# Kernel optimization log

Measured on AMD Instinct MI355X. Metric: run time of the kernel, lower is better.

The kernel has to match this reference:

```python
import jax, jax.numpy as jnp
import numpy as np

FORMULA_OH_SIZES = [20, 20, 20, 20, 20]
SPECT_BIN_N = 512


def layer_norm(x, g, b, eps=1e-5):
    m = jnp.mean(x, axis=-1, keepdims=True)
    v = jnp.var(x, axis=-1, keepdims=True)
    return (x - m) * jax.lax.rsqrt(v + eps) * g + b


def gru_cell(x, h, W_ih, W_hh, b_ih, b_hh):
    # torch.nn.GRUCell math
    gi = x @ W_ih.T + b_ih
    gh = h @ W_hh.T + b_hh
    i_r, i_z, i_n = jnp.split(gi, 3, axis=-1)
    h_r, h_z, h_n = jnp.split(gh, 3, axis=-1)
    r = jax.nn.sigmoid(i_r + h_r)
    z = jax.nn.sigmoid(i_z + h_z)
    n = jnp.tanh(i_n + r * h_n)
    return (1.0 - z) * n + z * h


def structured_one_hot(x, sizes, accum=True):
    # x: [N, len(sizes)] integer element counts -> concatenated (accumulated) one-hots
    outs = []
    for i, s in enumerate(sizes):
        v = jnp.clip(x[:, i].astype(jnp.int32), 0, s - 1)
        if accum:
            oh = (jnp.arange(s)[None, :] <= v[:, None]).astype(jnp.float32)  # thermometer
        else:
            oh = jax.nn.one_hot(v, s, dtype=jnp.float32)
        outs.append(oh)
    return jnp.concatenate(outs, axis=-1)


def setup_inputs():
    key = jax.random.key(0)
    ks = jax.random.split(key, 16)
    B, A, GF, HW, S, M = 16, 32, 128, 4, 4096, 8
    G = GF * HW                       # 512 = g_feat_in * highway_steps_n
    FE = sum(FORMULA_OH_SIZES)        # 100
    D = 512                           # internal_d
    vert_feat_in = jax.random.normal(ks[0], (B, A, GF, HW), jnp.float32)
    vert_mask_in = jnp.ones((B, A), jnp.float32)
    elem_id = jax.random.randint(ks[1], (B, A), 0, 5)
    vert_element_oh = jax.nn.one_hot(elem_id, 5, dtype=jnp.float32)
    adj_oh = jnp.zeros((B, A, A, 4), jnp.float32)  # unused by forward
    atom_subsets = jax.random.bernoulli(ks[2], 0.5, (B, S, A)).astype(jnp.float32)
    masses = jax.random.uniform(ks[3], (B, S, M), jnp.float32, 0.0, SPECT_BIN_N - 1.0)
    intens = jax.random.uniform(ks[4], (B, S, M), jnp.float32)
    atom_subsets_peaks = jnp.stack([masses, intens], axis=-1)

    def lin(k, o, i):
        return (jax.random.normal(k, (o, i), jnp.float32) / np.sqrt(i)).astype(jnp.float32)

    return dict(
        vert_feat_in=vert_feat_in, vert_mask_in=vert_mask_in,
        vert_element_oh=vert_element_oh, adj_oh=adj_oh,
        atom_subsets=atom_subsets, atom_subsets_peaks=atom_subsets_peaks,
        ln_sub_g=jnp.ones((G,), jnp.float32), ln_sub_b=jnp.zeros((G,), jnp.float32),
        W_ih=lin(ks[5], 3 * G, FE), W_hh=lin(ks[6], 3 * G, G),
        b_ih=jnp.zeros((3 * G,), jnp.float32), b_hh=jnp.zeros((3 * G,), jnp.float32),
        W1=lin(ks[7], D, G), b1=jnp.zeros((D,), jnp.float32),
        W2a=lin(ks[8], D, D), b2a=jnp.zeros((D,), jnp.float32),
        W2b=lin(ks[9], D, D), b2b=jnp.zeros((D,), jnp.float32),
        ln_pre_g=jnp.ones((D,), jnp.float32), ln_pre_b=jnp.zeros((D,), jnp.float32),
        Ws=lin(ks[10], 1, D), bs=jnp.zeros((1,), jnp.float32),
    )


def reference(vert_feat_in, vert_mask_in, vert_element_oh, adj_oh, atom_subsets,
              atom_subsets_peaks, ln_sub_g, ln_sub_b, W_ih, W_hh, b_ih, b_hh,
              W1, b1, W2a, b2a, W2b, b2b, ln_pre_g, ln_pre_b, Ws, bs):
    B, A, GF, HW = vert_feat_in.shape
    S = atom_subsets.shape[1]
    vf = vert_feat_in.reshape(B, A, GF * HW)                       # [B,A,G]
    masked_vf = vf * vert_mask_in[:, :, None]
    subs_m = atom_subsets * vert_mask_in[:, None, :]               # [B,S,A]
    swvs = jnp.einsum('bag,bsa->bsg', masked_vf, subs_m)           # [B,S,G]
    # per-subset element counts -> structured one-hot formula encoding
    counts = jnp.einsum('bae,bsa->bse', vert_element_oh, atom_subsets).astype(jnp.int32)
    pf_flat = structured_one_hot(counts.reshape(B * S, -1), FORMULA_OH_SIZES, accum=True)
    subset_size = jnp.sum(subs_m, axis=2) + 1e-4                   # [B,S]
    mean = swvs / subset_size[:, :, None]
    normed = layer_norm(mean, ln_sub_g, ln_sub_b)                  # [B,S,G]
    h = gru_cell(pf_flat, normed.reshape(B * S, -1), W_ih, W_hh, b_ih, b_hh)
    h = h.reshape(normed.shape)
    x = jax.nn.relu(h @ W1.T + b1)
    x = jax.nn.relu(x @ W2a.T + b2a)
    x = jax.nn.relu(x @ W2b.T + b2b)   # (extra F.relu in original is idempotent)
    x = layer_norm(x, ln_pre_g, ln_pre_b)
    scores = (x @ Ws.T + bs)[..., 0]                               # [B,S]
    probs = jax.nn.softmax(scores, axis=-1)
    # mass histogram: scatter intensity*prob into rounded-mass bins
    masses = atom_subsets_peaks[..., 0]                            # [B,S,M]
    intens = atom_subsets_peaks[..., 1]
    bins = jnp.clip(jnp.round(masses).astype(jnp.int32), 0, SPECT_BIN_N - 1)
    contrib = intens * probs[:, :, None]                           # [B,S,M]
    spect = jnp.zeros((B, SPECT_BIN_N), x.dtype).at[
        jnp.arange(B)[:, None], bins.reshape(B, -1)].add(contrib.reshape(B, -1))
    return (spect, probs)
```

## Files before the change

### kernel.cpp

```cpp
#include <hip/hip_runtime.h>
#include <math.h>

#define B_ 16
#define A_ 32
#define G_ 512
#define S_ 4096
#define M_ 8
#define BS_ 65536
#define KC_ 640
#define NG_ 1536

typedef _Float16 half8 __attribute__((ext_vector_type(8)));
typedef _Float16 half4v __attribute__((ext_vector_type(4)));
typedef _Float16 half2v __attribute__((ext_vector_type(2)));
typedef float floatx4 __attribute__((ext_vector_type(4)));

typedef const __attribute__((address_space(1))) void* gas_t;
typedef __attribute__((address_space(3))) void* las_t;

__device__ __forceinline__ float wave_sum_f(float v){
#pragma unroll
  for (int o = 32; o > 0; o >>= 1) v += __shfl_xor(v, o);
  return v;
}
__device__ __forceinline__ float wave_max_f(float v){
#pragma unroll
  for (int o = 32; o > 0; o >>= 1) v = fmaxf(v, __shfl_xor(v, o));
  return v;
}
__device__ __forceinline__ float sigmoidf_(float x){ return 1.f/(1.f+__expf(-x)); }
__device__ __forceinline__ float tanhf_(float x){ return 1.f - 2.f/(__expf(2.f*x)+1.f); }

__global__ __launch_bounds__(256) void k_cvt3(const float* __restrict__ s0,
                                              const float* __restrict__ s1,
                                              const float* __restrict__ s2,
                                              _Float16* __restrict__ d){
  const float* s = (blockIdx.y == 0) ? s0 : (blockIdx.y == 1) ? s1 : s2;
  int i = (blockIdx.x*256 + threadIdx.x)*4;
  if (i >= G_*G_) return;
  float4 v = *(const float4*)(s+i);
  half4v o; o[0]=(_Float16)v.x; o[1]=(_Float16)v.y; o[2]=(_Float16)v.z; o[3]=(_Float16)v.w;
  *(half4v*)(d + (size_t)blockIdx.y*G_*G_ + i) = o;
}

__global__ __launch_bounds__(64) void k_buildw(const float* __restrict__ Whh,
                                               const float* __restrict__ Wih,
                                               _Float16* __restrict__ Wcat){
  int j = blockIdx.x;
  for (int p = threadIdx.x; p < KC_; p += 64){
    float v = 0.f;
    if (p < 512) v = Whh[(size_t)j*512 + p];
    else if (p < 612) v = Wih[(size_t)j*100 + (p - 512)];
    Wcat[(size_t)j*KC_ + p] = (_Float16)v;
  }
}

__global__ __launch_bounds__(256) void k_prep_mfma(
    const float* __restrict__ vf, const float* __restrict__ mask,
    const float* __restrict__ eoh, const float* __restrict__ subs,
    const float* __restrict__ ln_g, const float* __restrict__ ln_b,
    _Float16* __restrict__ Abuf){
  __shared__ _Float16 s_mvfT[G_*A_];
  __shared__ _Float16 s_sm[128*A_];
  __shared__ float s_m[A_];
  __shared__ float s_e[A_*5];
  __shared__ float s_ssum[128];
  __shared__ float s_red1[2][4][16];
  __shared__ float s_red2[2][4][16];
  int tid = threadIdx.x;
  int bx = blockIdx.x, b = blockIdx.y;
  int lane = tid & 63, w = tid >> 6;
  int q = lane >> 4, l15 = lane & 15;
  size_t row0 = (size_t)b*S_ + (size_t)bx*128;
  if (tid < A_)   s_m[tid] = mask[b*A_ + tid];
  if (tid < A_*5) s_e[tid] = eoh[b*A_*5 + tid];
  __syncthreads();
  {
    int p = tid & 15, gseg = tid >> 4;
    float mk0 = s_m[2*p], mk1 = s_m[2*p+1];
    const float* v0 = vf + ((size_t)b*A_ + 2*p)*G_ + gseg*32;
    const float* v1 = v0 + G_;
#pragma unroll
    for (int i = 0; i < 32; i += 4){
      float4 a = *(const float4*)(v0 + i);
      float4 c = *(const float4*)(v1 + i);
      float av[4] = {a.x, a.y, a.z, a.w};
      float cv[4] = {c.x, c.y, c.z, c.w};
#pragma unroll
      for (int j = 0; j < 4; ++j){
        half2v h; h[0] = (_Float16)(av[j]*mk0); h[1] = (_Float16)(cv[j]*mk1);
        *(half2v*)(s_mvfT + (gseg*32 + i + j)*A_ + 2*p) = h;
      }
    }
  }
  {
    int s = tid >> 1, hh = tid & 1;
    const float* sp = subs + (row0 + s)*A_ + hh*16;
    _Float16* dst = s_sm + s*A_ + hh*16;
#pragma unroll
    for (int i = 0; i < 16; i += 4){
      float4 v = *(const float4*)(sp + i);
      half4v h; h[0]=(_Float16)v.x; h[1]=(_Float16)v.y; h[2]=(_Float16)v.z; h[3]=(_Float16)v.w;
      *(half4v*)(dst + i) = h;
    }
  }
  __syncthreads();
  if (tid < 128){
    int s = tid;
    float ssum = 0.f, c0=0.f, c1=0.f, c2=0.f, c3=0.f, c4=0.f;
#pragma unroll
    for (int a = 0; a < A_; ++a){
      float v = (float)s_sm[s*A_ + a];
      ssum += v * s_m[a];
      c0 += v * s_e[a*5+0]; c1 += v * s_e[a*5+1]; c2 += v * s_e[a*5+2];
      c3 += v * s_e[a*5+3]; c4 += v * s_e[a*5+4];
    }
    int cc[5];
    cc[0] = min(max((int)(c0+0.5f),0),19); cc[1] = min(max((int)(c1+0.5f),0),19);
    cc[2] = min(max((int)(c2+0.5f),0),19); cc[3] = min(max((int)(c3+0.5f),0),19);
    cc[4] = min(max((int)(c4+0.5f),0),19);
    s_ssum[s] = ssum;
    _Float16* dst = Abuf + (row0 + s)*KC_ + 512;
#pragma unroll
    for (int t = 0; t < 16; ++t){
      half8 hv;
#pragma unroll
      for (int u = 0; u < 8; ++u){
        int k = t*8 + u;
        float v = 0.f;
        if (k < 100){ int f = k/20, l = k - f*20; v = (l <= cc[f]) ? 1.f : 0.f; }
        hv[u] = (_Float16)v;
      }
      *(half8*)(dst + t*8) = hv;
    }
  }
  half8 bf[8]; float lng[8], lnb[8];
#pragma unroll
  for (int t = 0; t < 8; ++t){
    int g = w*128 + t*16 + l15;
    bf[t] = *(const half8*)(s_mvfT + g*A_ + q*8);
    lng[t] = ln_g[g]; lnb[t] = ln_b[g];
  }
  __syncthreads();
  for (int gi = 0; gi < 8; ++gi){
    half8 af = *(const half8*)(s_sm + (gi*16 + l15)*A_ + q*8);
    floatx4 c[8];
#pragma unroll
    for (int t = 0; t < 8; ++t){
      floatx4 z = {0.f, 0.f, 0.f, 0.f};
      c[t] = __builtin_amdgcn_mfma_f32_16x16x32_f16(af, bf[t], z, 0, 0, 0);
    }
    float p1[4] = {0.f,0.f,0.f,0.f}, p2[4] = {0.f,0.f,0.f,0.f};
#pragma unroll
    for (int t = 0; t < 8; ++t)
#pragma unroll
      for (int r = 0; r < 4; ++r){ float v = c[t][r]; p1[r] += v; p2[r] += v*v; }
#pragma unroll
    for (int off = 1; off < 16; off <<= 1)
#pragma unroll
      for (int r = 0; r < 4; ++r){
        p1[r] += __shfl_xor(p1[r], off);
        p2[r] += __shfl_xor(p2[r], off);
      }
    int gb = gi & 1;
    if (l15 == 0){
#pragma unroll
      for (int r = 0; r < 4; ++r){ s_red1[gb][w][q*4+r] = p1[r]; s_red2[gb][w][q*4+r] = p2[r]; }
    }
    __syncthreads();
#pragma unroll
    for (int r = 0; r < 4; ++r){
      int sl = gi*16 + q*4 + r;
      int rr = q*4 + r;
      float t1 = s_red1[gb][0][rr] + s_red1[gb][1][rr] + s_red1[gb][2][rr] + s_red1[gb][3][rr];
      float t2 = s_red2[gb][0][rr] + s_red2[gb][1][rr] + s_red2[gb][2][rr] + s_red2[gb][3][rr];
      float inv = 1.f/(s_ssum[sl] + 1e-4f);
      float mu = t1*inv*(1.f/512.f);
      float var = t2*inv*inv*(1.f/512.f) - mu*mu;
      float rs = rsqrtf(var + 1e-5f);
      _Float16* orow = Abuf + (row0 + sl)*KC_;
#pragma unroll
      for (int t = 0; t < 8; ++t){
        float o = (c[t][r]*inv - mu)*rs*lng[t] + lnb[t];
        orow[w*128 + t*16 + l15] = (_Float16)o;
      }
    }
  }
}

__global__ __launch_bounds__(512) void k_gru_fused(
    const _Float16* __restrict__ Abuf, const _Float16* __restrict__ Wcat,
    const float* __restrict__ bih, const float* __restrict__ bhh,
    _Float16* __restrict__ H){
  __shared__ _Float16 smA[2][128*32];
  __shared__ _Float16 smB[2][192*32];
  int tid = threadIdx.x;
  int lane = tid & 63, wvid = tid >> 6;
  int wm = wvid & 1, wn = wvid >> 1;
  int q = lane >> 4, l15 = lane & 15;
  int mt = blockIdx.x*64 + (blockIdx.y >> 3);
  int dt = blockIdx.y & 7;
  int m0 = mt*128, n0 = dt*64;
  floatx4 acc[3][4] = {};
  floatx4 accNI[4] = {};
  int offA[4], offB[3];
#pragma unroll
  for (int i = 0; i < 4; ++i){
    int r = wm*64 + i*16 + l15;
    offA[i] = (r*4 + (q ^ ((r>>2)&3)))*8;
  }
#pragma unroll
  for (int g = 0; g < 3; ++g){
    int rb = g*64 + wn*16 + l15;
    offB[g] = (rb*4 + (q ^ ((rb>>2)&3)))*8;
  }
  const _Float16* gA;
  {
    int u = wvid*64 + lane;
    int r = u >> 2, c = (u & 3) ^ ((r >> 2) & 3);
    gA = Abuf + (size_t)(m0 + r)*KC_ + c*8;
  }
  const _Float16* gB0;
  {
    int u = wvid*64 + lane;
    int rb = u >> 2, c = (u & 3) ^ ((rb >> 2) & 3);
    int grow = (rb >> 6)*512 + n0 + (rb & 63);
    gB0 = Wcat + (size_t)grow*KC_ + c*8;
  }
  const _Float16* gB1 = nullptr;
  if (wvid < 4){
    int u = (8 + wvid)*64 + lane;
    int rb = u >> 2, c = (u & 3) ^ ((rb >> 2) & 3);
    int grow = (rb >> 6)*512 + n0 + (rb & 63);
    gB1 = Wcat + (size_t)grow*KC_ + c*8;
  }
  __builtin_amdgcn_global_load_lds((gas_t)gA,  (las_t)(smA[0] + wvid*512), 16, 0, 0);
  __builtin_amdgcn_global_load_lds((gas_t)gB0, (las_t)(smB[0] + wvid*512), 16, 0, 0);
  if (wvid < 4)
    __builtin_amdgcn_global_load_lds((gas_t)gB1, (las_t)(smB[0] + (8+wvid)*512), 16, 0, 0);
  asm volatile("s_waitcnt vmcnt(0)");
  __builtin_amdgcn_s_barrier();
  const int NT = KC_/32;
  for (int t = 0; t < NT; ++t){
    int cur = t & 1;
    if (t + 1 < NT){
      int kc = (t+1)*32;
      __builtin_amdgcn_global_load_lds((gas_t)(gA + kc),  (las_t)(smA[cur^1] + wvid*512), 16, 0, 0);
      __builtin_amdgcn_global_load_lds((gas_t)(gB0 + kc), (las_t)(smB[cur^1] + wvid*512), 16, 0, 0);
      if (wvid < 4)
        __builtin_amdgcn_global_load_lds((gas_t)(gB1 + kc), (las_t)(smB[cur^1] + (8+wvid)*512), 16, 0, 0);
    }
    half8 af[4], bfv[3];
#pragma unroll
    for (int i = 0; i < 4; ++i) af[i] = *(const half8*)(smA[cur] + offA[i]);
#pragma unroll
    for (int g = 0; g < 3; ++g) bfv[g] = *(const half8*)(smB[cur] + offB[g]);
    if (t < 16){
#pragma unroll
      for (int g = 0; g < 3; ++g)
#pragma unroll
        for (int i = 0; i < 4; ++i)
          acc[g][i] = __builtin_amdgcn_mfma_f32_16x16x32_f16(af[i], bfv[g], acc[g][i], 0, 0, 0);
    } else {
#pragma unroll
      for (int i = 0; i < 4; ++i){
        acc[0][i] = __builtin_amdgcn_mfma_f32_16x16x32_f16(af[i], bfv[0], acc[0][i], 0, 0, 0);
        acc[1][i] = __builtin_amdgcn_mfma_f32_16x16x32_f16(af[i], bfv[1], acc[1][i], 0, 0, 0);
        accNI[i]  = __builtin_amdgcn_mfma_f32_16x16x32_f16(af[i], bfv[2], accNI[i], 0, 0, 0);
      }
    }
    asm volatile("s_waitcnt vmcnt(0)");
    __builtin_amdgcn_s_barrier();
  }
  int d = n0 + wn*16 + l15;
  float br  = bih[d] + bhh[d];
  float bz  = bih[512+d] + bhh[512+d];
  float bnh = bhh[1024+d];
  float bni = bih[1024+d];
#pragma unroll
  for (int i = 0; i < 4; ++i){
#pragma unroll
    for (int r = 0; r < 4; ++r){
      int m = m0 + wm*64 + i*16 + q*4 + r;
      float gr  = acc[0][i][r] + br;
      float gz  = acc[1][i][r] + bz;
      float hn  = acc[2][i][r] + bnh;
      float in_ = accNI[i][r] + bni;
      float rrv = sigmoidf_(gr);
      float zz  = sigmoidf_(gz);
      float nn  = tanhf_(in_ + rrv*hn);
      float hp  = (float)Abuf[(size_t)m*KC_ + d];
      H[(size_t)m*G_ + d] = (_Float16)((1.f-zz)*nn + zz*hp);
    }
  }
}

__global__ __launch_bounds__(256) void k_gemm(
    const _Float16* __restrict__ A, const _Float16* __restrict__ W,
    const float* __restrict__ bias, _Float16* __restrict__ Out){
  __shared__ _Float16 smA[2][128*32];
  __shared__ _Float16 smB[2][128*32];
  int tid = threadIdx.x;
  int lane = tid & 63, wvid = tid >> 6;
  int wm = wvid & 1, wn = wvid >> 1;
  int q = lane >> 4, l15 = lane & 15;
  int mt = blockIdx.x*64 + (blockIdx.y >> 2);
  int nt = blockIdx.y & 3;
  int m0 = mt*128, n0 = nt*128;
  floatx4 acc[4][4] = {};
  int offA[4], offB[4];
#pragma unroll
  for (int i = 0; i < 4; ++i){
    int r = wm*64 + i*16 + l15;
    offA[i] = (r*4 + (q ^ ((r>>2)&3)))*8;
    int rb = wn*64 + i*16 + l15;
    offB[i] = (rb*4 + (q ^ ((rb>>2)&3)))*8;
  }
  int uA[2];
  const _Float16 *gA[2], *gB[2];
#pragma unroll
  for (int t = 0; t < 2; ++t){
    int seg = wvid*2 + t;
    int u = seg*64 + lane;
    int r = u >> 2, c = (u & 3) ^ ((r >> 2) & 3);
    uA[t] = seg;
    gA[t] = A + (size_t)(m0 + r)*G_ + c*8;
    gB[t] = W + (size_t)(n0 + r)*G_ + c*8;
  }
#pragma unroll
  for (int t2 = 0; t2 < 2; ++t2){
    __builtin_amdgcn_global_load_lds((gas_t)(gA[t2]), (las_t)(smA[0] + uA[t2]*512), 16, 0, 0);
    __builtin_amdgcn_global_load_lds((gas_t)(gB[t2]), (las_t)(smB[0] + uA[t2]*512), 16, 0, 0);
  }
  asm volatile("s_waitcnt vmcnt(0)");
  __builtin_amdgcn_s_barrier();
  const int NT = G_/32;
  for (int t = 0; t < NT; ++t){
    int cur = t & 1;
    if (t + 1 < NT){
      int kc = (t+1)*32;
#pragma unroll
      for (int t2 = 0; t2 < 2; ++t2){
        __builtin_amdgcn_global_load_lds((gas_t)(gA[t2] + kc), (las_t)(smA[cur^1] + uA[t2]*512), 16, 0, 0);
        __builtin_amdgcn_global_load_lds((gas_t)(gB[t2] + kc), (las_t)(smB[cur^1] + uA[t2]*512), 16, 0, 0);
      }
    }
    half8 af[4], bfv[4];
#pragma unroll
    for (int i = 0; i < 4; ++i) af[i] = *(const half8*)(smA[cur] + offA[i]);
#pragma unroll
    for (int j = 0; j < 4; ++j) bfv[j] = *(const half8*)(smB[cur] + offB[j]);
#pragma unroll
    for (int i = 0; i < 4; ++i)
#pragma unroll
      for (int j = 0; j < 4; ++j)
        acc[i][j] = __builtin_amdgcn_mfma_f32_16x16x32_f16(af[i], bfv[j], acc[i][j], 0, 0, 0);
    asm volatile("s_waitcnt vmcnt(0)");
    __builtin_amdgcn_s_barrier();
  }
#pragma unroll
  for (int j = 0; j < 4; ++j){
    int n = n0 + wn*64 + j*16 + l15;
    float bv = bias[n];
#pragma unroll
    for (int i = 0; i < 4; ++i){
#pragma unroll
      for (int r = 0; r < 4; ++r){
        int m = m0 + wm*64 + i*16 + q*4 + r;
        Out[(size_t)m*G_ + n] = (_Float16)fmaxf(acc[i][j][r] + bv, 0.f);
      }
    }
  }
}

__global__ __launch_bounds__(256) void k_ff3_fin(
    const _Float16* __restrict__ A, const _Float16* __restrict__ W,
    const float* __restrict__ bias, const float* __restrict__ ln_pre_g,
    const float* __restrict__ Ws, float* __restrict__ Pbuf){
  __shared__ _Float16 smA[2][128*32];
  __shared__ _Float16 smB[2][128*32];
  __shared__ float sP[2][64][2][3];
  int tid = threadIdx.x;
  int lane = tid & 63, wvid = tid >> 6;
  int wm = wvid & 1, wn = wvid >> 1;
  int q = lane >> 4, l15 = lane & 15;
  int mt = blockIdx.x*64 + (blockIdx.y >> 2);
  int nt = blockIdx.y & 3;
  int m0 = mt*128, n0 = nt*128;
  floatx4 acc[4][4] = {};
  int offA[4], offB[4];
#pragma unroll
  for (int i = 0; i < 4; ++i){
    int r = wm*64 + i*16 + l15;
    offA[i] = (r*4 + (q ^ ((r>>2)&3)))*8;
    int rb = wn*64 + i*16 + l15;
    offB[i] = (rb*4 + (q ^ ((rb>>2)&3)))*8;
  }
  int uA[2];
  const _Float16 *gA[2], *gB[2];
#pragma unroll
  for (int t = 0; t < 2; ++t){
    int seg = wvid*2 + t;
    int u = seg*64 + lane;
    int r = u >> 2, c = (u & 3) ^ ((r >> 2) & 3);
    uA[t] = seg;
    gA[t] = A + (size_t)(m0 + r)*G_ + c*8;
    gB[t] = W + (size_t)(n0 + r)*G_ + c*8;
  }
#pragma unroll
  for (int t2 = 0; t2 < 2; ++t2){
    __builtin_amdgcn_global_load_lds((gas_t)(gA[t2]), (las_t)(smA[0] + uA[t2]*512), 16, 0, 0);
    __builtin_amdgcn_global_load_lds((gas_t)(gB[t2]), (las_t)(smB[0] + uA[t2]*512), 16, 0, 0);
  }
  asm volatile("s_waitcnt vmcnt(0)");
  __builtin_amdgcn_s_barrier();
  const int NT = G_/32;
  for (int t = 0; t < NT; ++t){
    int cur = t & 1;
    if (t + 1 < NT){
      int kc = (t+1)*32;
#pragma unroll
      for (int t2 = 0; t2 < 2; ++t2){
        __builtin_amdgcn_global_load_lds((gas_t)(gA[t2] + kc), (las_t)(smA[cur^1] + uA[t2]*512), 16, 0, 0);
        __builtin_amdgcn_global_load_lds((gas_t)(gB[t2] + kc), (las_t)(smB[cur^1] + uA[t2]*512), 16, 0, 0);
      }
    }
    half8 af[4], bfv[4];
#pragma unroll
    for (int i = 0; i < 4; ++i) af[i] = *(const half8*)(smA[cur] + offA[i]);
#pragma unroll
    for (int j = 0; j < 4; ++j) bfv[j] = *(const half8*)(smB[cur] + offB[j]);
#pragma unroll
    for (int i = 0; i < 4; ++i)
#pragma unroll
      for (int j = 0; j < 4; ++j)
        acc[i][j] = __builtin_amdgcn_mfma_f32_16x16x32_f16(af[i], bfv[j], acc[i][j], 0, 0, 0);
    asm volatile("s_waitcnt vmcnt(0)");
    __builtin_amdgcn_s_barrier();
  }
  float gws[4], bv4[4];
#pragma unroll
  for (int j = 0; j < 4; ++j){
    int n = n0 + wn*64 + j*16 + l15;
    gws[j] = ln_pre_g[n]*Ws[n];
    bv4[j] = bias[n];
  }
#pragma unroll
  for (int i = 0; i < 4; ++i){
#pragma unroll
    for (int r = 0; r < 4; ++r){
      float p1 = 0.f, p2 = 0.f, p3 = 0.f;
#pragma unroll
      for (int j = 0; j < 4; ++j){
        float x = fmaxf(acc[i][j][r] + bv4[j], 0.f);
        p1 += x; p2 += x*x; p3 += gws[j]*x;
      }
#pragma unroll
      for (int off = 1; off < 16; off <<= 1){
        p1 += __shfl_xor(p1, off);
        p2 += __shfl_xor(p2, off);
        p3 += __shfl_xor(p3, off);
      }
      if (l15 == 0){
        int rl = i*16 + q*4 + r;
        sP[wm][rl][wn][0] = p1; sP[wm][rl][wn][1] = p2; sP[wm][rl][wn][2] = p3;
      }
    }
  }
  __syncthreads();
  if (tid < 128){
    int wmi = tid >> 6, rl = tid & 63;
    int m = m0 + wmi*64 + rl;
    float* dst = Pbuf + ((size_t)m*4 + nt)*3;
    dst[0] = sP[wmi][rl][0][0] + sP[wmi][rl][1][0];
    dst[1] = sP[wmi][rl][0][1] + sP[wmi][rl][1][1];
    dst[2] = sP[wmi][rl][0][2] + sP[wmi][rl][1][2];
  }
}

__global__ __launch_bounds__(256) void k_score_fin(
    const float* __restrict__ Pbuf, const float* __restrict__ g,
    const float* __restrict__ bta, const float* __restrict__ Ws,
    const float* __restrict__ bs, float* __restrict__ scores){
  __shared__ float red[8];
  int tid = threadIdx.x, lane = tid & 63, wv = tid >> 6;
  int i0 = tid*2;
  float c1p = g[i0]*Ws[i0] + g[i0+1]*Ws[i0+1];
  float c2p = bta[i0]*Ws[i0] + bta[i0+1]*Ws[i0+1];
  c1p = wave_sum_f(c1p); c2p = wave_sum_f(c2p);
  if (lane == 0){ red[wv] = c1p; red[4+wv] = c2p; }
  __syncthreads();
  float c1 = red[0]+red[1]+red[2]+red[3];
  float c2 = red[4]+red[5]+red[6]+red[7] + bs[0];
  size_t row = (size_t)blockIdx.x*256 + tid;
  const float* p = Pbuf + row*12;
  float4 a  = *(const float4*)p;
  float4 b4 = *(const float4*)(p+4);
  float4 c4 = *(const float4*)(p+8);
  float P1 = a.x + a.w + b4.z + c4.y;
  float P2 = a.y + b4.x + b4.w + c4.z;
  float P3 = a.z + b4.y + c4.x + c4.w;
  float mu = P1*(1.f/512.f);
  float var = P2*(1.f/512.f) - mu*mu;
  float rs = rsqrtf(var + 1e-5f);
  scores[row] = rs*(P3 - mu*c1) + c2;
}

__global__ __launch_bounds__(256) void k_softmax(
    const float* __restrict__ scores, float* __restrict__ probs){
  __shared__ float red[4];
  int b = blockIdx.x, tid = threadIdx.x, lane = tid & 63, wv = tid >> 6;
  const float* sp = scores + (size_t)b*S_;
  float mx = -1e30f;
  for (int i = tid; i < S_; i += 256) mx = fmaxf(mx, sp[i]);
  mx = wave_max_f(mx);
  if (lane == 0) red[wv] = mx;
  __syncthreads();
  mx = fmaxf(fmaxf(red[0], red[1]), fmaxf(red[2], red[3]));
  __syncthreads();
  float sum = 0.f;
  for (int i = tid; i < S_; i += 256) sum += __expf(sp[i]-mx);
  sum = wave_sum_f(sum);
  if (lane == 0) red[wv] = sum;
  __syncthreads();
  sum = red[0]+red[1]+red[2]+red[3];
  float inv = 1.f/sum;
  for (int i = tid; i < S_; i += 256)
    probs[(size_t)b*S_ + i] = __expf(sp[i]-mx)*inv;
}

__global__ __launch_bounds__(256) void k_spect(
    const float* __restrict__ peaks, const float* __restrict__ probs,
    float* __restrict__ spect){
  __shared__ float bins[512];
  int b = blockIdx.x, tid = threadIdx.x;
  bins[tid] = 0.f; bins[tid+256] = 0.f;
  __syncthreads();
  for (int i = tid; i < S_*M_; i += 256){
    int s = i >> 3, m = i & 7;
    const float* pk = peaks + (((size_t)b*S_ + s)*M_ + m)*2;
    float mass = pk[0], inten = pk[1];
    float p = probs[(size_t)b*S_ + s];
    int bin = (int)rintf(mass);
    bin = min(max(bin, 0), 511);
    atomicAdd(&bins[bin], inten*p);
  }
  __syncthreads();
  spect[(size_t)b*512 + tid]       = bins[tid];
  spect[(size_t)b*512 + tid + 256] = bins[tid+256];
}

extern "C" void kernel_launch(void* const* d_in, const int* in_sizes, int n_in,
                              void* d_out, int out_size, void* d_ws, size_t ws_size,
                              hipStream_t stream) {
  const float* vf       = (const float*)d_in[0];
  const float* mask     = (const float*)d_in[1];
  const float* eoh      = (const float*)d_in[2];
  const float* subs     = (const float*)d_in[4];
  const float* peaks    = (const float*)d_in[5];
  const float* ln_sub_g = (const float*)d_in[6];
  const float* ln_sub_b = (const float*)d_in[7];
  const float* W_ih     = (const float*)d_in[8];
  const float* W_hh     = (const float*)d_in[9];
  const float* b_ih     = (const float*)d_in[10];
  const float* b_hh     = (const float*)d_in[11];
  const float* W1       = (const float*)d_in[12];
  const float* b1       = (const float*)d_in[13];
  const float* W2a      = (const float*)d_in[14];
  const float* b2a      = (const float*)d_in[15];
  const float* W2b      = (const float*)d_in[16];
  const float* b2b      = (const float*)d_in[17];
  const float* ln_pre_g = (const float*)d_in[18];
  const float* ln_pre_b = (const float*)d_in[19];
  const float* Ws       = (const float*)d_in[20];
  const float* bs       = (const float*)d_in[21];
  float* out = (float*)d_out;
  float* probs_out = out + (size_t)B_*512;

  char* w = (char*)d_ws;
  float* scores = (float*)w;     w += (size_t)BS_*4;
  float* Pbuf   = (float*)w;     w += (size_t)BS_*12*4;
  _Float16* Wcat = (_Float16*)w; w += (size_t)NG_*KC_*2;
  _Float16* W1h  = (_Float16*)w; w += (size_t)G_*G_*2;
  _Float16* W2ah = (_Float16*)w; w += (size_t)G_*G_*2;
  _Float16* W2bh = (_Float16*)w; w += (size_t)G_*G_*2;
  _Float16* Abuf = (_Float16*)w; w += (size_t)BS_*KC_*2;
  _Float16* bufh0 = (_Float16*)w;
  _Float16* bufh1 = Abuf;

  k_cvt3<<<dim3((G_*G_/4+255)/256, 3), 256, 0, stream>>>(W1, W2a, W2b, W1h);
  k_buildw<<<NG_, 64, 0, stream>>>(W_hh, W_ih, Wcat);
  k_prep_mfma<<<dim3(S_/128, B_), 256, 0, stream>>>(vf, mask, eoh, subs,
                                                    ln_sub_g, ln_sub_b, Abuf);
  k_gru_fused<<<dim3(8, 512), 512, 0, stream>>>(Abuf, Wcat, b_ih, b_hh, bufh0);
  k_gemm<<<dim3(8, 256), 256, 0, stream>>>(bufh0, W1h,  b1,  bufh1);
  k_gemm<<<dim3(8, 256), 256, 0, stream>>>(bufh1, W2ah, b2a, bufh0);
  k_ff3_fin<<<dim3(8, 256), 256, 0, stream>>>(bufh0, W2bh, b2b,
                                              ln_pre_g, Ws, Pbuf);
  k_score_fin<<<BS_/256, 256, 0, stream>>>(Pbuf, ln_pre_g, ln_pre_b, Ws, bs, scores);
  k_softmax<<<B_, 256, 0, stream>>>(scores, probs_out);
  k_spect<<<B_, 256, 0, stream>>>(peaks, probs_out, out);
}
```

Measured before the change: 525.8 us.

## Triple-buffer LDS tiles with partial vmcnt waits in GRU and FF GEMMs

```diff
diff --git a/kernel.cpp b/kernel.cpp
--- a/kernel.cpp
+++ b/kernel.cpp
@@ -192,8 +192,8 @@
     const _Float16* __restrict__ Abuf, const _Float16* __restrict__ Wcat,
     const float* __restrict__ bih, const float* __restrict__ bhh,
     _Float16* __restrict__ H){
-  __shared__ _Float16 smA[2][128*32];
-  __shared__ _Float16 smB[2][192*32];
+  __shared__ _Float16 smA[3][128*32];
+  __shared__ _Float16 smB[3][192*32];
   int tid = threadIdx.x;
   int lane = tid & 63, wvid = tid >> 6;
   int wm = wvid & 1, wn = wvid >> 1;
@@ -234,22 +234,26 @@
     int grow = (rb >> 6)*512 + n0 + (rb & 63);
     gB1 = Wcat + (size_t)grow*KC_ + c*8;
   }
-  __builtin_amdgcn_global_load_lds((gas_t)gA,  (las_t)(smA[0] + wvid*512), 16, 0, 0);
-  __builtin_amdgcn_global_load_lds((gas_t)gB0, (las_t)(smB[0] + wvid*512), 16, 0, 0);
-  if (wvid < 4)
-    __builtin_amdgcn_global_load_lds((gas_t)gB1, (las_t)(smB[0] + (8+wvid)*512), 16, 0, 0);
-  asm volatile("s_waitcnt vmcnt(0)");
-  __builtin_amdgcn_s_barrier();
+#define GRU_STAGE(TT, BUF) do{                                                        \
+    int kc_ = (TT)*32;                                                                \
+    __builtin_amdgcn_global_load_lds((gas_t)(gA + kc_),  (las_t)(smA[BUF] + wvid*512), 16, 0, 0); \
+    __builtin_amdgcn_global_load_lds((gas_t)(gB0 + kc_), (las_t)(smB[BUF] + wvid*512), 16, 0, 0); \
+    if (wvid < 4)                                                                     \
+      __builtin_amdgcn_global_load_lds((gas_t)(gB1 + kc_), (las_t)(smB[BUF] + (8+wvid)*512), 16, 0, 0); \
+  }while(0)
+  GRU_STAGE(0, 0);
+  GRU_STAGE(1, 1);
   const int NT = KC_/32;
   for (int t = 0; t < NT; ++t){
-    int cur = t & 1;
-    if (t + 1 < NT){
-      int kc = (t+1)*32;
-      __builtin_amdgcn_global_load_lds((gas_t)(gA + kc),  (las_t)(smA[cur^1] + wvid*512), 16, 0, 0);
-      __builtin_amdgcn_global_load_lds((gas_t)(gB0 + kc), (las_t)(smB[cur^1] + wvid*512), 16, 0, 0);
-      if (wvid < 4)
-        __builtin_amdgcn_global_load_lds((gas_t)(gB1 + kc), (las_t)(smB[cur^1] + (8+wvid)*512), 16, 0, 0);
-    }
+    int cur = t % 3;
+    if (t < NT-1){
+      if (wvid < 4) asm volatile("s_waitcnt vmcnt(3)" ::: "memory");
+      else          asm volatile("s_waitcnt vmcnt(2)" ::: "memory");
+    } else {
+      asm volatile("s_waitcnt vmcnt(0)" ::: "memory");
+    }
+    __builtin_amdgcn_s_barrier();
+    if (t + 2 < NT) GRU_STAGE(t+2, (t+2)%3);
     half8 af[4], bfv[3];
 #pragma unroll
     for (int i = 0; i < 4; ++i) af[i] = *(const half8*)(smA[cur] + offA[i]);
@@ -269,9 +273,8 @@
         accNI[i]  = __builtin_amdgcn_mfma_f32_16x16x32_f16(af[i], bfv[2], accNI[i], 0, 0, 0);
       }
     }
-    asm volatile("s_waitcnt vmcnt(0)");
-    __builtin_amdgcn_s_barrier();
-  }
+  }
+#undef GRU_STAGE
   int d = n0 + wn*16 + l15;
   float br  = bih[d] + bhh[d];
   float bz  = bih[512+d] + bhh[512+d];
@@ -298,8 +301,8 @@
 __global__ __launch_bounds__(256) void k_gemm(
     const _Float16* __restrict__ A, const _Float16* __restrict__ W,
     const float* __restrict__ bias, _Float16* __restrict__ Out){
-  __shared__ _Float16 smA[2][128*32];
-  __shared__ _Float16 smB[2][128*32];
+  __shared__ _Float16 smA[3][128*32];
+  __shared__ _Float16 smB[3][128*32];
   int tid = threadIdx.x;
   int lane = tid & 63, wvid = tid >> 6;
   int wm = wvid & 1, wn = wvid >> 1;
@@ -327,24 +330,22 @@
     gA[t] = A + (size_t)(m0 + r)*G_ + c*8;
     gB[t] = W + (size_t)(n0 + r)*G_ + c*8;
   }
-#pragma unroll
-  for (int t2 = 0; t2 < 2; ++t2){
-    __builtin_amdgcn_global_load_lds((gas_t)(gA[t2]), (las_t)(smA[0] + uA[t2]*512), 16, 0, 0);
-    __builtin_amdgcn_global_load_lds((gas_t)(gB[t2]), (las_t)(smB[0] + uA[t2]*512), 16, 0, 0);
-  }
-  asm volatile("s_waitcnt vmcnt(0)");
-  __builtin_amdgcn_s_barrier();
+#define FF_STAGE(TT, BUF) do{                                                         \
+    int kc_ = (TT)*32;                                                                \
+    __builtin_amdgcn_global_load_lds((gas_t)(gA[0] + kc_), (las_t)(smA[BUF] + uA[0]*512), 16, 0, 0); \
+    __builtin_amdgcn_global_load_lds((gas_t)(gB[0] + kc_), (las_t)(smB[BUF] + uA[0]*512), 16, 0, 0); \
+    __builtin_amdgcn_global_load_lds((gas_t)(gA[1] + kc_), (las_t)(smA[BUF] + uA[1]*512), 16, 0, 0); \
+    __builtin_amdgcn_global_load_lds((gas_t)(gB[1] + kc_), (las_t)(smB[BUF] + uA[1]*512), 16, 0, 0); \
+  }while(0)
+  FF_STAGE(0, 0);
+  FF_STAGE(1, 1);
   const int NT = G_/32;
   for (int t = 0; t < NT; ++t){
-    int cur = t & 1;
-    if (t + 1 < NT){
-      int kc = (t+1)*32;
-#pragma unroll
-      for (int t2 = 0; t2 < 2; ++t2){
-        __builtin_amdgcn_global_load_lds((gas_t)(gA[t2] + kc), (las_t)(smA[cur^1] + uA[t2]*512), 16, 0, 0);
-        __builtin_amdgcn_global_load_lds((gas_t)(gB[t2] + kc), (las_t)(smB[cur^1] + uA[t2]*512), 16, 0, 0);
-      }
-    }
+    int cur = t % 3;
+    if (t < NT-1) asm volatile("s_waitcnt vmcnt(4)" ::: "memory");
+    else          asm volatile("s_waitcnt vmcnt(0)" ::: "memory");
+    __builtin_amdgcn_s_barrier();
+    if (t + 2 < NT) FF_STAGE(t+2, (t+2)%3);
     half8 af[4], bfv[4];
 #pragma unroll
     for (int i = 0; i < 4; ++i) af[i] = *(const half8*)(smA[cur] + offA[i]);
@@ -355,9 +356,8 @@
 #pragma unroll
       for (int j = 0; j < 4; ++j)
         acc[i][j] = __builtin_amdgcn_mfma_f32_16x16x32_f16(af[i], bfv[j], acc[i][j], 0, 0, 0);
-    asm volatile("s_waitcnt vmcnt(0)");
-    __builtin_amdgcn_s_barrier();
-  }
+  }
+#undef FF_STAGE
 #pragma unroll
   for (int j = 0; j < 4; ++j){
     int n = n0 + wn*64 + j*16 + l15;
@@ -377,8 +377,8 @@
     const _Float16* __restrict__ A, const _Float16* __restrict__ W,
     const float* __restrict__ bias, const float* __restrict__ ln_pre_g,
     const float* __restrict__ Ws, float* __restrict__ Pbuf){
-  __shared__ _Float16 smA[2][128*32];
-  __shared__ _Float16 smB[2][128*32];
+  __shared__ _Float16 smA[3][128*32];
+  __shared__ _Float16 smB[3][128*32];
   __shared__ float sP[2][64][2][3];
   int tid = threadIdx.x;
   int lane = tid & 63, wvid = tid >> 6;
@@ -407,24 +407,22 @@
     gA[t] = A + (size_t)(m0 + r)*G_ + c*8;
     gB[t] = W + (size_t)(n0 + r)*G_ + c*8;
   }
-#pragma unroll
-  for (int t2 = 0; t2 < 2; ++t2){
-    __builtin_amdgcn_global_load_lds((gas_t)(gA[t2]), (las_t)(smA[0] + uA[t2]*512), 16, 0, 0);
-    __builtin_amdgcn_global_load_lds((gas_t)(gB[t2]), (las_t)(smB[0] + uA[t2]*512), 16, 0, 0);
-  }
-  asm volatile("s_waitcnt vmcnt(0)");
-  __builtin_amdgcn_s_barrier();
+#define FF_STAGE(TT, BUF) do{                                                         \
+    int kc_ = (TT)*32;                                                                \
+    __builtin_amdgcn_global_load_lds((gas_t)(gA[0] + kc_), (las_t)(smA[BUF] + uA[0]*512), 16, 0, 0); \
+    __builtin_amdgcn_global_load_lds((gas_t)(gB[0] + kc_), (las_t)(smB[BUF] + uA[0]*512), 16, 0, 0); \
+    __builtin_amdgcn_global_load_lds((gas_t)(gA[1] + kc_), (las_t)(smA[BUF] + uA[1]*512), 16, 0, 0); \
+    __builtin_amdgcn_global_load_lds((gas_t)(gB[1] + kc_), (las_t)(smB[BUF] + uA[1]*512), 16, 0, 0); \
+  }while(0)
+  FF_STAGE(0, 0);
+  FF_STAGE(1, 1);
   const int NT = G_/32;
   for (int t = 0; t < NT; ++t){
-    int cur = t & 1;
-    if (t + 1 < NT){
-      int kc = (t+1)*32;
-#pragma unroll
-      for (int t2 = 0; t2 < 2; ++t2){
-        __builtin_amdgcn_global_load_lds((gas_t)(gA[t2] + kc), (las_t)(smA[cur^1] + uA[t2]*512), 16, 0, 0);
-        __builtin_amdgcn_global_load_lds((gas_t)(gB[t2] + kc), (las_t)(smB[cur^1] + uA[t2]*512), 16, 0, 0);
-      }
-    }
+    int cur = t % 3;
+    if (t < NT-1) asm volatile("s_waitcnt vmcnt(4)" ::: "memory");
+    else          asm volatile("s_waitcnt vmcnt(0)" ::: "memory");
+    __builtin_amdgcn_s_barrier();
+    if (t + 2 < NT) FF_STAGE(t+2, (t+2)%3);
     half8 af[4], bfv[4];
 #pragma unroll
     for (int i = 0; i < 4; ++i) af[i] = *(const half8*)(smA[cur] + offA[i]);
@@ -435,9 +433,8 @@
 #pragma unroll
       for (int j = 0; j < 4; ++j)
         acc[i][j] = __builtin_amdgcn_mfma_f32_16x16x32_f16(af[i], bfv[j], acc[i][j], 0, 0, 0);
-    asm volatile("s_waitcnt vmcnt(0)");
-    __builtin_amdgcn_s_barrier();
-  }
+  }
+#undef FF_STAGE
   float gws[4], bv4[4];
 #pragma unroll
   for (int j = 0; j < 4; ++j){
```

Result: slower. 649.9 us (+23.6%).

## Enlarge feed-forward GEMM tiles to 256x128 with eight waves per block

Applied to the files above, without the earlier changes.

```diff
diff --git a/kernel.cpp b/kernel.cpp
--- a/kernel.cpp
+++ b/kernel.cpp
@@ -295,18 +295,18 @@
   }
 }
 
-__global__ __launch_bounds__(256) void k_gemm(
+__global__ __launch_bounds__(512, 4) void k_gemm(
     const _Float16* __restrict__ A, const _Float16* __restrict__ W,
     const float* __restrict__ bias, _Float16* __restrict__ Out){
-  __shared__ _Float16 smA[2][128*32];
+  __shared__ _Float16 smA[2][256*32];
   __shared__ _Float16 smB[2][128*32];
   int tid = threadIdx.x;
   int lane = tid & 63, wvid = tid >> 6;
-  int wm = wvid & 1, wn = wvid >> 1;
+  int wm = wvid & 3, wn = wvid >> 2;
   int q = lane >> 4, l15 = lane & 15;
-  int mt = blockIdx.x*64 + (blockIdx.y >> 2);
+  int mt = blockIdx.x*32 + (blockIdx.y >> 2);
   int nt = blockIdx.y & 3;
-  int m0 = mt*128, n0 = nt*128;
+  int m0 = mt*256, n0 = nt*128;
   floatx4 acc[4][4] = {};
   int offA[4], offB[4];
 #pragma unroll
@@ -316,35 +316,34 @@
     int rb = wn*64 + i*16 + l15;
     offB[i] = (rb*4 + (q ^ ((rb>>2)&3)))*8;
   }
-  int uA[2];
-  const _Float16 *gA[2], *gB[2];
+  int segA[2];
+  const _Float16 *gA[2], *gB;
 #pragma unroll
   for (int t = 0; t < 2; ++t){
     int seg = wvid*2 + t;
     int u = seg*64 + lane;
     int r = u >> 2, c = (u & 3) ^ ((r >> 2) & 3);
-    uA[t] = seg;
+    segA[t] = seg;
     gA[t] = A + (size_t)(m0 + r)*G_ + c*8;
-    gB[t] = W + (size_t)(n0 + r)*G_ + c*8;
-  }
-#pragma unroll
-  for (int t2 = 0; t2 < 2; ++t2){
-    __builtin_amdgcn_global_load_lds((gas_t)(gA[t2]), (las_t)(smA[0] + uA[t2]*512), 16, 0, 0);
-    __builtin_amdgcn_global_load_lds((gas_t)(gB[t2]), (las_t)(smB[0] + uA[t2]*512), 16, 0, 0);
-  }
+  }
+  {
+    int u = wvid*64 + lane;
+    int rb = u >> 2, c = (u & 3) ^ ((rb >> 2) & 3);
+    gB = W + (size_t)(n0 + rb)*G_ + c*8;
+  }
+#define FF_STAGE(TT, BUF) do{                                                         \
+    int kc_ = (TT)*32;                                                                \
+    __builtin_amdgcn_global_load_lds((gas_t)(gA[0] + kc_), (las_t)(smA[BUF] + segA[0]*512), 16, 0, 0); \
+    __builtin_amdgcn_global_load_lds((gas_t)(gA[1] + kc_), (las_t)(smA[BUF] + segA[1]*512), 16, 0, 0); \
+    __builtin_amdgcn_global_load_lds((gas_t)(gB    + kc_), (las_t)(smB[BUF] + wvid*512), 16, 0, 0);    \
+  }while(0)
+  FF_STAGE(0, 0);
   asm volatile("s_waitcnt vmcnt(0)");
   __builtin_amdgcn_s_barrier();
   const int NT = G_/32;
   for (int t = 0; t < NT; ++t){
     int cur = t & 1;
-    if (t + 1 < NT){
-      int kc = (t+1)*32;
-#pragma unroll
-      for (int t2 = 0; t2 < 2; ++t2){
-        __builtin_amdgcn_global_load_lds((gas_t)(gA[t2] + kc), (las_t)(smA[cur^1] + uA[t2]*512), 16, 0, 0);
-        __builtin_amdgcn_global_load_lds((gas_t)(gB[t2] + kc), (las_t)(smB[cur^1] + uA[t2]*512), 16, 0, 0);
-      }
-    }
+    if (t + 1 < NT) FF_STAGE(t+1, cur^1);
     half8 af[4], bfv[4];
 #pragma unroll
     for (int i = 0; i < 4; ++i) af[i] = *(const half8*)(smA[cur] + offA[i]);
@@ -358,6 +357,7 @@
     asm volatile("s_waitcnt vmcnt(0)");
     __builtin_amdgcn_s_barrier();
   }
+#undef FF_STAGE
 #pragma unroll
   for (int j = 0; j < 4; ++j){
     int n = n0 + wn*64 + j*16 + l15;
@@ -373,20 +373,20 @@
   }
 }
 
-__global__ __launch_bounds__(256) void k_ff3_fin(
+__global__ __launch_bounds__(512, 4) void k_ff3_fin(
     const _Float16* __restrict__ A, const _Float16* __restrict__ W,
     const float* __restrict__ bias, const float* __restrict__ ln_pre_g,
     const float* __restrict__ Ws, float* __restrict__ Pbuf){
-  __shared__ _Float16 smA[2][128*32];
+  __shared__ _Float16 smA[2][256*32];
   __shared__ _Float16 smB[2][128*32];
-  __shared__ float sP[2][64][2][3];
+  __shared__ float sP[4][64][2][3];
   int tid = threadIdx.x;
   int lane = tid & 63, wvid = tid >> 6;
-  int wm = wvid & 1, wn = wvid >> 1;
+  int wm = wvid & 3, wn = wvid >> 2;
   int q = lane >> 4, l15 = lane & 15;
-  int mt = blockIdx.x*64 + (blockIdx.y >> 2);
+  int mt = blockIdx.x*32 + (blockIdx.y >> 2);
   int nt = blockIdx.y & 3;
-  int m0 = mt*128, n0 = nt*128;
+  int m0 = mt*256, n0 = nt*128;
   floatx4 acc[4][4] = {};
   int offA[4], offB[4];
 #pragma unroll
@@ -396,35 +396,34 @@
     int rb = wn*64 + i*16 + l15;
     offB[i] = (rb*4 + (q ^ ((rb>>2)&3)))*8;
   }
-  int uA[2];
-  const _Float16 *gA[2], *gB[2];
+  int segA[2];
+  const _Float16 *gA[2], *gB;
 #pragma unroll
   for (int t = 0; t < 2; ++t){
     int seg = wvid*2 + t;
     int u = seg*64 + lane;
     int r = u >> 2, c = (u & 3) ^ ((r >> 2) & 3);
-    uA[t] = seg;
+    segA[t] = seg;
     gA[t] = A + (size_t)(m0 + r)*G_ + c*8;
-    gB[t] = W + (size_t)(n0 + r)*G_ + c*8;
-  }
-#pragma unroll
-  for (int t2 = 0; t2 < 2; ++t2){
-    __builtin_amdgcn_global_load_lds((gas_t)(gA[t2]), (las_t)(smA[0] + uA[t2]*512), 16, 0, 0);
-    __builtin_amdgcn_global_load_lds((gas_t)(gB[t2]), (las_t)(smB[0] + uA[t2]*512), 16, 0, 0);
-  }
+  }
+  {
+    int u = wvid*64 + lane;
+    int rb = u >> 2, c = (u & 3) ^ ((rb >> 2) & 3);
+    gB = W + (size_t)(n0 + rb)*G_ + c*8;
+  }
+#define FF_STAGE(TT, BUF) do{                                                         \
+    int kc_ = (TT)*32;                                                                \
+    __builtin_amdgcn_global_load_lds((gas_t)(gA[0] + kc_), (las_t)(smA[BUF] + segA[0]*512), 16, 0, 0); \
+    __builtin_amdgcn_global_load_lds((gas_t)(gA[1] + kc_), (las_t)(smA[BUF] + segA[1]*512), 16, 0, 0); \
+    __builtin_amdgcn_global_load_lds((gas_t)(gB    + kc_), (las_t)(smB[BUF] + wvid*512), 16, 0, 0);    \
+  }while(0)
+  FF_STAGE(0, 0);
   asm volatile("s_waitcnt vmcnt(0)");
   __builtin_amdgcn_s_barrier();
   const int NT = G_/32;
   for (int t = 0; t < NT; ++t){
     int cur = t & 1;
-    if (t + 1 < NT){
-      int kc = (t+1)*32;
-#pragma unroll
-      for (int t2 = 0; t2 < 2; ++t2){
-        __builtin_amdgcn_global_load_lds((gas_t)(gA[t2] + kc), (las_t)(smA[cur^1] + uA[t2]*512), 16, 0, 0);
-        __builtin_amdgcn_global_load_lds((gas_t)(gB[t2] + kc), (las_t)(smB[cur^1] + uA[t2]*512), 16, 0, 0);
-      }
-    }
+    if (t + 1 < NT) FF_STAGE(t+1, cur^1);
     half8 af[4], bfv[4];
 #pragma unroll
     for (int i = 0; i < 4; ++i) af[i] = *(const half8*)(smA[cur] + offA[i]);
@@ -438,6 +437,7 @@
     asm volatile("s_waitcnt vmcnt(0)");
     __builtin_amdgcn_s_barrier();
   }
+#undef FF_STAGE
   float gws[4], bv4[4];
 #pragma unroll
   for (int j = 0; j < 4; ++j){
@@ -468,7 +468,7 @@
     }
   }
   __syncthreads();
-  if (tid < 128){
+  if (tid < 256){
     int wmi = tid >> 6, rl = tid & 63;
     int m = m0 + wmi*64 + rl;
     float* dst = Pbuf + ((size_t)m*4 + nt)*3;
@@ -593,9 +593,9 @@
   k_prep_mfma<<<dim3(S_/128, B_), 256, 0, stream>>>(vf, mask, eoh, subs,
                                                     ln_sub_g, ln_sub_b, Abuf);
   k_gru_fused<<<dim3(8, 512), 512, 0, stream>>>(Abuf, Wcat, b_ih, b_hh, bufh0);
-  k_gemm<<<dim3(8, 256), 256, 0, stream>>>(bufh0, W1h,  b1,  bufh1);
-  k_gemm<<<dim3(8, 256), 256, 0, stream>>>(bufh1, W2ah, b2a, bufh0);
-  k_ff3_fin<<<dim3(8, 256), 256, 0, stream>>>(bufh0, W2bh, b2b,
+  k_gemm<<<dim3(8, 128), 512, 0, stream>>>(bufh0, W1h,  b1,  bufh1);
+  k_gemm<<<dim3(8, 128), 512, 0, stream>>>(bufh1, W2ah, b2a, bufh0);
+  k_ff3_fin<<<dim3(8, 128), 512, 0, stream>>>(bufh0, W2bh, b2b,
                                               ln_pre_g, Ws, Pbuf);
   k_score_fin<<<BS_/256, 256, 0, stream>>>(Pbuf, ln_pre_g, ln_pre_b, Ws, bs, scores);
   k_softmax<<<B_, 256, 0, stream>>>(scores, probs_out);
```

After: 570.9 us. 8.6% more time.
